# Kernel optimization log

Measured on AMD Instinct MI355X. Metric: run time of the kernel, lower is better.

The kernel has to match this reference:

```python
import jax, jax.numpy as jnp
import numpy as np

B, T, D, H, HD, FF = 1024, 128, 128, 4, 32, 512
SCALE = D ** -0.5  # NOTE: original scales by full EMBED_DIM**-0.5, not head_dim
EPS = 1e-5


def setup_inputs() -> dict:
    key = jax.random.key(0)
    ks = jax.random.split(key, 14)
    s = 0.02
    return {
        "x": jax.random.normal(ks[0], (B, T, D), dtype=jnp.float32),
        "ln1_g": jnp.ones((D,), jnp.float32),
        "ln1_b": jnp.zeros((D,), jnp.float32),
        "Wq": jax.random.normal(ks[1], (H, HD, D), jnp.float32) * s,
        "Wk": jax.random.normal(ks[2], (H, HD, D), jnp.float32) * s,
        "Wv": jax.random.normal(ks[3], (H, HD, D), jnp.float32) * s,
        "Wo": jax.random.normal(ks[4], (D, D), jnp.float32) * s,
        "bo": jnp.zeros((D,), jnp.float32),
        "ln2_g": jnp.ones((D,), jnp.float32),
        "ln2_b": jnp.zeros((D,), jnp.float32),
        "W1": jax.random.normal(ks[5], (FF, D), jnp.float32) * s,
        "b1": jnp.zeros((FF,), jnp.float32),
        "W2": jax.random.normal(ks[6], (D, FF), jnp.float32) * s,
        "b2": jnp.zeros((D,), jnp.float32),
    }


def _layer_norm(x, g, b):
    mu = jnp.mean(x, axis=-1, keepdims=True)
    var = jnp.mean(jnp.square(x - mu), axis=-1, keepdims=True)
    return (x - mu) * jax.lax.rsqrt(var + EPS) * g + b


def reference(x, ln1_g, ln1_b, Wq, Wk, Wv, Wo, bo, ln2_g, ln2_b, W1, b1, W2, b2):
    # --- attention sub-block ---
    h = _layer_norm(x, ln1_g, ln1_b)                       # [B,T,D]
    q = jnp.einsum('btd,nhd->bnth', h, Wq)                 # [B,H,T,HD]
    k = jnp.einsum('btd,nhd->bnth', h, Wk)
    v = jnp.einsum('btd,nhd->bnth', h, Wv)
    scores = jnp.einsum('bnth,bnsh->bnts', q, k) * SCALE   # [B,H,T,T]
    causal = jnp.tril(jnp.ones((T, T), dtype=bool))
    scores = jnp.where(causal, scores, -jnp.inf)
    w = jax.nn.softmax(scores, axis=-1)                    # dropout = eval identity
    attn = jnp.einsum('bnts,bnsh->bnth', w, v)             # [B,H,T,HD]
    attn = attn.transpose(0, 2, 1, 3).reshape(B, T, D)     # concat heads
    x = x + attn @ Wo.T + bo
    # --- feed-forward sub-block ---
    h2 = _layer_norm(x, ln2_g, ln2_b)
    ff = jax.nn.relu(h2 @ W1.T + b1) @ W2.T + b2
    return x + ff
```

## Files before the change

### kernel.cpp

```cpp
#include <hip/hip_runtime.h>
#include <hip/hip_bf16.h>


typedef short bf16x8 __attribute__((ext_vector_type(8)));
typedef float f32x4  __attribute__((ext_vector_type(4)));
typedef unsigned short u16;
typedef unsigned int   u32;

#define TT   128
#define DDIM 128
#define FFD  512
#define PIT  136

__device__ __forceinline__ u16 f2b(float f) {
    __hip_bfloat16 h = __float2bfloat16(f);
    return __builtin_bit_cast(u16, h);
}
__device__ __forceinline__ bf16x8 ldfrag(const u16* p) {
    return __builtin_bit_cast(bf16x8, *reinterpret_cast<const uint4*>(p));
}
__device__ __forceinline__ bf16x8 ldfrag_f32(const float* p) {
    float4 a = *reinterpret_cast<const float4*>(p);
    float4 b = *reinterpret_cast<const float4*>(p + 4);
    bf16x8 r;
    r[0] = (short)f2b(a.x); r[1] = (short)f2b(a.y);
    r[2] = (short)f2b(a.z); r[3] = (short)f2b(a.w);
    r[4] = (short)f2b(b.x); r[5] = (short)f2b(b.y);
    r[6] = (short)f2b(b.z); r[7] = (short)f2b(b.w);
    return r;
}
__device__ __forceinline__ f32x4 mfma16(bf16x8 a, bf16x8 b, f32x4 c) {
    return __builtin_amdgcn_mfma_f32_16x16x32_bf16(a, b, c, 0, 0, 0);
}

__global__ __launch_bounds__(512, 2) void tblock_kernel(
    const float* __restrict__ x,
    const float* __restrict__ ln1g, const float* __restrict__ ln1b,
    const float* __restrict__ Wq,   const float* __restrict__ Wk, const float* __restrict__ Wv,
    const float* __restrict__ Wo,   const float* __restrict__ bo,
    const float* __restrict__ ln2g, const float* __restrict__ ln2b,
    const float* __restrict__ W1,   const float* __restrict__ b1,
    const float* __restrict__ W2,   const float* __restrict__ b2,
    float* __restrict__ out)
{
    __shared__ __align__(16) u16 sm[4 * TT * PIT];
    u16* bufA = sm;
    u16* bufB = sm + 1 * TT * PIT;
    u16* bufC = sm + 2 * TT * PIT;
    u16* bufD = sm + 3 * TT * PIT;

    const int b    = blockIdx.x;
    const int tid  = threadIdx.x;
    const int w    = tid >> 6;
    const int l    = tid & 63;
    const int lq   = l & 15;
    const int quad = l >> 4;
    const float* xb = x + (size_t)b * (TT * DDIM);

    {
        const int row = tid >> 2, part = tid & 3;
        const float* src = xb + row * DDIM + part * 32;
        float v[32];
        float s = 0.f, s2 = 0.f;
        #pragma unroll
        for (int i = 0; i < 8; i++) {
            float4 u = *reinterpret_cast<const float4*>(src + i * 4);
            v[i * 4 + 0] = u.x; v[i * 4 + 1] = u.y;
            v[i * 4 + 2] = u.z; v[i * 4 + 3] = u.w;
            s  += u.x + u.y + u.z + u.w;
            s2 += u.x * u.x + u.y * u.y + u.z * u.z + u.w * u.w;
        }
        s  += __shfl_xor(s, 1);  s2 += __shfl_xor(s2, 1);
        s  += __shfl_xor(s, 2);  s2 += __shfl_xor(s2, 2);
        float mean = s * (1.f / 128.f);
        float var  = fmaxf(s2 * (1.f / 128.f) - mean * mean, 0.f);
        float rstd = rsqrtf(var + 1e-5f);
        u16* dst = bufA + row * PIT + part * 32;
        #pragma unroll
        for (int i = 0; i < 4; i++) {
            u32 o4[4];
            #pragma unroll
            for (int j = 0; j < 4; j++) {
                int c = part * 32 + i * 8 + 2 * j;
                float r0 = (v[i * 8 + 2 * j]     - mean) * rstd * ln1g[c]     + ln1b[c];
                float r1 = (v[i * 8 + 2 * j + 1] - mean) * rstd * ln1g[c + 1] + ln1b[c + 1];
                o4[j] = (u32)f2b(r0) | ((u32)f2b(r1) << 16);
            }
            uint4 pk; pk.x = o4[0]; pk.y = o4[1]; pk.z = o4[2]; pk.w = o4[3];
            *reinterpret_cast<uint4*>(dst + i * 8) = pk;
        }
    }
    __syncthreads();

    {
        bf16x8 bq[4], bk[4];
        #pragma unroll
        for (int ks = 0; ks < 4; ks++) {
            bq[ks] = ldfrag_f32(Wq + (w * 16 + lq) * DDIM + ks * 32 + quad * 8);
            bk[ks] = ldfrag_f32(Wk + (w * 16 + lq) * DDIM + ks * 32 + quad * 8);
        }
        #pragma unroll
        for (int m = 0; m < 8; m++) {
            f32x4 accq = {0, 0, 0, 0}, acck = {0, 0, 0, 0};
            #pragma unroll
            for (int ks = 0; ks < 4; ks++) {
                bf16x8 a = ldfrag(bufA + (m * 16 + lq) * PIT + ks * 32 + quad * 8);
                accq = mfma16(a, bq[ks], accq);
                acck = mfma16(a, bk[ks], acck);
            }
            #pragma unroll
            for (int r = 0; r < 4; r++) {
                int t = m * 16 + quad * 4 + r;
                bufB[t * PIT + w * 16 + lq] = f2b(accq[r]);
                bufC[t * PIT + w * 16 + lq] = f2b(acck[r]);
            }
        }
        bf16x8 av[4];
        #pragma unroll
        for (int ks = 0; ks < 4; ks++)
            av[ks] = ldfrag_f32(Wv + (w * 16 + lq) * DDIM + ks * 32 + quad * 8);
        #pragma unroll
        for (int n = 0; n < 8; n++) {
            f32x4 acc = {0, 0, 0, 0};
            #pragma unroll
            for (int ks = 0; ks < 4; ks++) {
                bf16x8 bh = ldfrag(bufA + (n * 16 + lq) * PIT + ks * 32 + quad * 8);
                acc = mfma16(av[ks], bh, acc);
            }
            #pragma unroll
            for (int r = 0; r < 4; r++) {
                int o = w * 16 + quad * 4 + r;
                bufD[o * PIT + n * 16 + lq] = f2b(acc[r]);
            }
        }
    }
    __syncthreads();

    const float SCALE = 0.08838834764831845f;
    #pragma unroll 1
    for (int h = 0; h < 4; h++) {
        bf16x8 aq = ldfrag(bufB + (w * 16 + lq) * PIT + h * 32 + quad * 8);
        float p[8][4];
        #pragma unroll
        for (int n = 0; n < 8; n++) {
            bf16x8 bk = ldfrag(bufC + (n * 16 + lq) * PIT + h * 32 + quad * 8);
            f32x4 s4 = {0, 0, 0, 0};
            s4 = mfma16(aq, bk, s4);
            #pragma unroll
            for (int r = 0; r < 4; r++) p[n][r] = s4[r];
        }
        #pragma unroll
        for (int r = 0; r < 4; r++) {
            int t = w * 16 + quad * 4 + r;
            float mx = -3.0e38f;
            #pragma unroll
            for (int n = 0; n < 8; n++) {
                int sc = n * 16 + lq;
                float val = p[n][r] * SCALE;
                p[n][r] = val;
                mx = (sc <= t) ? fmaxf(mx, val) : mx;
            }
            mx = fmaxf(mx, __shfl_xor(mx, 1));
            mx = fmaxf(mx, __shfl_xor(mx, 2));
            mx = fmaxf(mx, __shfl_xor(mx, 4));
            mx = fmaxf(mx, __shfl_xor(mx, 8));
            float sum = 0.f;
            #pragma unroll
            for (int n = 0; n < 8; n++) {
                int sc = n * 16 + lq;
                float e = (sc <= t) ? __expf(p[n][r] - mx) : 0.f;
                p[n][r] = e; sum += e;
            }
            sum += __shfl_xor(sum, 1);
            sum += __shfl_xor(sum, 2);
            sum += __shfl_xor(sum, 4);
            sum += __shfl_xor(sum, 8);
            float inv = 1.f / sum;
            #pragma unroll
            for (int n = 0; n < 8; n++)
                bufA[t * PIT + n * 16 + lq] = f2b(p[n][r] * inv);
        }
        __syncthreads();
        f32x4 o0 = {0, 0, 0, 0}, o1 = {0, 0, 0, 0};
        #pragma unroll
        for (int ks = 0; ks < 4; ks++) {
            bf16x8 ap  = ldfrag(bufA + (w * 16 + lq) * PIT + ks * 32 + quad * 8);
            bf16x8 bv0 = ldfrag(bufD + (h * 32 + lq) * PIT + ks * 32 + quad * 8);
            bf16x8 bv1 = ldfrag(bufD + (h * 32 + 16 + lq) * PIT + ks * 32 + quad * 8);
            o0 = mfma16(ap, bv0, o0);
            o1 = mfma16(ap, bv1, o1);
        }
        __syncthreads();
        #pragma unroll
        for (int r = 0; r < 4; r++) {
            int t = w * 16 + quad * 4 + r;
            bufB[t * PIT + h * 32 + lq]      = f2b(o0[r]);
            bufB[t * PIT + h * 32 + 16 + lq] = f2b(o1[r]);
        }
    }
    __syncthreads();

    float x1res[8][4];
    const int dcol = w * 16 + lq;
    {
        bf16x8 bw[4];
        #pragma unroll
        for (int ks = 0; ks < 4; ks++)
            bw[ks] = ldfrag_f32(Wo + (w * 16 + lq) * DDIM + ks * 32 + quad * 8);
        const float bov = bo[dcol];
        #pragma unroll
        for (int m = 0; m < 8; m++) {
            f32x4 acc = {0, 0, 0, 0};
            #pragma unroll
            for (int ks = 0; ks < 4; ks++) {
                bf16x8 a = ldfrag(bufB + (m * 16 + lq) * PIT + ks * 32 + quad * 8);
                acc = mfma16(a, bw[ks], acc);
            }
            #pragma unroll
            for (int r = 0; r < 4; r++) {
                int t = m * 16 + quad * 4 + r;
                float xv = xb[t * DDIM + dcol];
                float x1 = acc[r] + xv + bov;
                x1res[m][r] = x1;
                bufC[t * PIT + dcol] = f2b(x1);
            }
        }
    }
    __syncthreads();

    {
        const int row = tid >> 2, part = tid & 3;
        const u16* src = bufC + row * PIT + part * 32;
        float v[32];
        float s = 0.f, s2 = 0.f;
        #pragma unroll
        for (int i = 0; i < 4; i++) {
            uint4 u = *reinterpret_cast<const uint4*>(src + i * 8);
            u32 arr[4] = {u.x, u.y, u.z, u.w};
            #pragma unroll
            for (int j = 0; j < 4; j++) {
                float f0 = __uint_as_float((arr[j] & 0xffffu) << 16);
                float f1 = __uint_as_float(arr[j] & 0xffff0000u);
                v[i * 8 + 2 * j] = f0; v[i * 8 + 2 * j + 1] = f1;
                s += f0 + f1; s2 += f0 * f0 + f1 * f1;
            }
        }
        s  += __shfl_xor(s, 1);  s2 += __shfl_xor(s2, 1);
        s  += __shfl_xor(s, 2);  s2 += __shfl_xor(s2, 2);
        float mean = s * (1.f / 128.f);
        float var  = fmaxf(s2 * (1.f / 128.f) - mean * mean, 0.f);
        float rstd = rsqrtf(var + 1e-5f);
        u16* dst = bufD + row * PIT + part * 32;
        #pragma unroll
        for (int i = 0; i < 4; i++) {
            u32 o4[4];
            #pragma unroll
            for (int j = 0; j < 4; j++) {
                int c = part * 32 + i * 8 + 2 * j;
                float r0 = (v[i * 8 + 2 * j]     - mean) * rstd * ln2g[c]     + ln2b[c];
                float r1 = (v[i * 8 + 2 * j + 1] - mean) * rstd * ln2g[c + 1] + ln2b[c + 1];
                o4[j] = (u32)f2b(r0) | ((u32)f2b(r1) << 16);
            }
            uint4 pk; pk.x = o4[0]; pk.y = o4[1]; pk.z = o4[2]; pk.w = o4[3];
            *reinterpret_cast<uint4*>(dst + i * 8) = pk;
        }
    }
    __syncthreads();

    f32x4 oacc[8];
    #pragma unroll
    for (int m = 0; m < 8; m++) oacc[m] = f32x4{0, 0, 0, 0};

    #pragma unroll 1
    for (int fc = 0; fc < 4; fc++) {
        const int fbase = fc * 128;
        bf16x8 wf1[4];
        #pragma unroll
        for (int ks = 0; ks < 4; ks++)
            wf1[ks] = ldfrag_f32(W1 + (fbase + w * 16 + lq) * DDIM + ks * 32 + quad * 8);
        const float b1v = b1[fbase + w * 16 + lq];
        #pragma unroll
        for (int m = 0; m < 8; m++) {
            f32x4 acc = {0, 0, 0, 0};
            #pragma unroll
            for (int ks = 0; ks < 4; ks++) {
                bf16x8 a = ldfrag(bufD + (m * 16 + lq) * PIT + ks * 32 + quad * 8);
                acc = mfma16(a, wf1[ks], acc);
            }
            #pragma unroll
            for (int r = 0; r < 4; r++) {
                int t = m * 16 + quad * 4 + r;
                float g = acc[r] + b1v;
                g = g > 0.f ? g : 0.f;
                bufA[t * PIT + w * 16 + lq] = f2b(g);
            }
        }
        __syncthreads();
        bf16x8 wf2[4];
        #pragma unroll
        for (int ks = 0; ks < 4; ks++)
            wf2[ks] = ldfrag_f32(W2 + (w * 16 + lq) * FFD + fbase + ks * 32 + quad * 8);
        #pragma unroll
        for (int m = 0; m < 8; m++) {
            #pragma unroll
            for (int ks = 0; ks < 4; ks++) {
                bf16x8 a = ldfrag(bufA + (m * 16 + lq) * PIT + ks * 32 + quad * 8);
                oacc[m] = mfma16(a, wf2[ks], oacc[m]);
            }
        }
        __syncthreads();
    }

    {
        const float b2v = b2[dcol];
        float* ob = out + (size_t)b * (TT * DDIM);
        #pragma unroll
        for (int m = 0; m < 8; m++) {
            #pragma unroll
            for (int r = 0; r < 4; r++) {
                int t = m * 16 + quad * 4 + r;
                ob[t * DDIM + dcol] = oacc[m][r] + x1res[m][r] + b2v;
            }
        }
    }
}

extern "C" void kernel_launch(void* const* d_in, const int* in_sizes, int n_in,
                              void* d_out, int out_size, void* d_ws, size_t ws_size,
                              hipStream_t stream) {
    const float* x    = (const float*)d_in[0];
    const float* ln1g = (const float*)d_in[1];
    const float* ln1b = (const float*)d_in[2];
    const float* Wq   = (const float*)d_in[3];
    const float* Wk   = (const float*)d_in[4];
    const float* Wv   = (const float*)d_in[5];
    const float* Wo   = (const float*)d_in[6];
    const float* bo   = (const float*)d_in[7];
    const float* ln2g = (const float*)d_in[8];
    const float* ln2b = (const float*)d_in[9];
    const float* W1   = (const float*)d_in[10];
    const float* b1   = (const float*)d_in[11];
    const float* W2   = (const float*)d_in[12];
    const float* b2   = (const float*)d_in[13];
    float* out = (float*)d_out;

    const int nblocks = in_sizes[0] / (TT * DDIM);
    tblock_kernel<<<dim3(nblocks), dim3(512), 0, stream>>>(
        x, ln1g, ln1b, Wq, Wk, Wv, Wo, bo, ln2g, ln2b, W1, b1, W2, b2, out);
}
```

Measured before the change: 325.6 us.

## Restructure attention per-head with register-resident Q, swizzled LDS, and fused Wo

Shrinks shared memory from four padded 128x136 buffers to 64KB, using XOR-swizzled layouts instead of padding, and raises launch bounds to target more blocks per CU. Q is computed once and held in registers through a shuffle-based fragment transpose. K and V are computed per head into small LDS tiles, and the Wo projection is fused into the head loop so the concatenated attention output never goes to LDS. Softmax now uses exp2 with a prescaled Q and a hardware reciprocal, and LN2 runs directly from accumulator registers. The cost is recomputing the h fragment loads and reloading weights from global each head, plus extra shuffles and more register pressure.

```diff
diff --git a/kernel.cpp b/kernel.cpp
--- a/kernel.cpp
+++ b/kernel.cpp
@@ -10,11 +10,32 @@
 #define TT   128
 #define DDIM 128
 #define FFD  512
-#define PIT  136
+#define KPIT 40
+
+#define QSCALE 0.12751743f
+
+#if defined(__has_builtin)
+#if __has_builtin(__builtin_amdgcn_exp2f)
+#define EXP2F(x) __builtin_amdgcn_exp2f(x)
+#else
+#define EXP2F(x) exp2f(x)
+#endif
+#if __has_builtin(__builtin_amdgcn_rcpf)
+#define RCPF(x) __builtin_amdgcn_rcpf(x)
+#else
+#define RCPF(x) (1.0f / (x))
+#endif
+#else
+#define EXP2F(x) exp2f(x)
+#define RCPF(x) (1.0f / (x))
+#endif
 
 __device__ __forceinline__ u16 f2b(float f) {
     __hip_bfloat16 h = __float2bfloat16(f);
     return __builtin_bit_cast(u16, h);
+}
+__device__ __forceinline__ u32 pk2(float x, float y) {
+    return (u32)f2b(x) | ((u32)f2b(y) << 16);
 }
 __device__ __forceinline__ bf16x8 ldfrag(const u16* p) {
     return __builtin_bit_cast(bf16x8, *reinterpret_cast<const uint4*>(p));
@@ -32,8 +53,42 @@
 __device__ __forceinline__ f32x4 mfma16(bf16x8 a, bf16x8 b, f32x4 c) {
     return __builtin_amdgcn_mfma_f32_16x16x32_bf16(a, b, c, 0, 0, 0);
 }
-
-__global__ __launch_bounds__(512, 2) void tblock_kernel(
+__device__ __forceinline__ bf16x8 ld_sw(const u16* base, int row, int cg) {
+    return ldfrag(base + row * 128 + ((cg ^ (row & 7)) * 8));
+}
+__device__ __forceinline__ void st_sw(u16* base, int row, int col, u16 v) {
+    base[row * 128 + (((col >> 3) ^ (row & 7)) * 8) + (col & 7)] = v;
+}
+
+__device__ __forceinline__ void quad_collect(const float (&vals)[8][4],
+                                             bf16x8 (&fr)[4], int lane) {
+    const int srcA = (lane & 15) + ((lane & 16) << 1);
+    const int srcB = srcA + 16;
+    const bool hi = (lane & 32) != 0;
+    #pragma unroll
+    for (int g = 0; g < 4; g++) {
+        u32 D00 = pk2(vals[2*g][0],     vals[2*g][1]);
+        u32 D01 = pk2(vals[2*g][2],     vals[2*g][3]);
+        u32 D10 = pk2(vals[2*g + 1][0], vals[2*g + 1][1]);
+        u32 D11 = pk2(vals[2*g + 1][2], vals[2*g + 1][3]);
+        u32 a00 = (u32)__shfl((int)D00, srcA);
+        u32 a10 = (u32)__shfl((int)D10, srcA);
+        u32 a01 = (u32)__shfl((int)D01, srcA);
+        u32 a11 = (u32)__shfl((int)D11, srcA);
+        u32 b00 = (u32)__shfl((int)D00, srcB);
+        u32 b10 = (u32)__shfl((int)D10, srcB);
+        u32 b01 = (u32)__shfl((int)D01, srcB);
+        u32 b11 = (u32)__shfl((int)D11, srcB);
+        uint4 q;
+        q.x = hi ? a10 : a00;
+        q.y = hi ? a11 : a01;
+        q.z = hi ? b10 : b00;
+        q.w = hi ? b11 : b01;
+        fr[g] = __builtin_bit_cast(bf16x8, q);
+    }
+}
+
+__global__ __launch_bounds__(512, 4) void tblock_kernel(
     const float* __restrict__ x,
     const float* __restrict__ ln1g, const float* __restrict__ ln1b,
     const float* __restrict__ Wq,   const float* __restrict__ Wk, const float* __restrict__ Wv,
@@ -43,11 +98,12 @@
     const float* __restrict__ W2,   const float* __restrict__ b2,
     float* __restrict__ out)
 {
-    __shared__ __align__(16) u16 sm[4 * TT * PIT];
-    u16* bufA = sm;
-    u16* bufB = sm + 1 * TT * PIT;
-    u16* bufC = sm + 2 * TT * PIT;
-    u16* bufD = sm + 3 * TT * PIT;
+    __shared__ __align__(16) u16 sm[32768];
+    u16* bufH = sm;
+    u16* r2   = sm + 16384;
+    u16* Kh   = r2;
+    u16* Vth  = r2 + 5120;
+    u16* bnc  = r2 + 5120 + 4096;
 
     const int b    = blockIdx.x;
     const int tid  = threadIdx.x;
@@ -75,7 +131,6 @@
         float mean = s * (1.f / 128.f);
         float var  = fmaxf(s2 * (1.f / 128.f) - mean * mean, 0.f);
         float rstd = rsqrtf(var + 1e-5f);
-        u16* dst = bufA + row * PIT + part * 32;
         #pragma unroll
         for (int i = 0; i < 4; i++) {
             u32 o4[4];
@@ -86,190 +141,190 @@
                 float r1 = (v[i * 8 + 2 * j + 1] - mean) * rstd * ln1g[c + 1] + ln1b[c + 1];
                 o4[j] = (u32)f2b(r0) | ((u32)f2b(r1) << 16);
             }
-            uint4 pk; pk.x = o4[0]; pk.y = o4[1]; pk.z = o4[2]; pk.w = o4[3];
-            *reinterpret_cast<uint4*>(dst + i * 8) = pk;
+            uint4 pkv; pkv.x = o4[0]; pkv.y = o4[1]; pkv.z = o4[2]; pkv.w = o4[3];
+            int g = (part * 4 + i) ^ (row & 7);
+            *reinterpret_cast<uint4*>(bufH + row * 128 + g * 8) = pkv;
         }
     }
     __syncthreads();
 
+    bf16x8 qf0, qf1, qf2, qf3;
     {
-        bf16x8 bq[4], bk[4];
-        #pragma unroll
-        for (int ks = 0; ks < 4; ks++) {
-            bq[ks] = ldfrag_f32(Wq + (w * 16 + lq) * DDIM + ks * 32 + quad * 8);
-            bk[ks] = ldfrag_f32(Wk + (w * 16 + lq) * DDIM + ks * 32 + quad * 8);
-        }
-        #pragma unroll
-        for (int m = 0; m < 8; m++) {
-            f32x4 accq = {0, 0, 0, 0}, acck = {0, 0, 0, 0};
+        bf16x8 hf[4];
+        #pragma unroll
+        for (int ks = 0; ks < 4; ks++) hf[ks] = ld_sw(bufH, w * 16 + lq, ks * 4 + quad);
+        float qt[8][4];
+        #pragma unroll
+        for (int mt = 0; mt < 8; mt++) {
+            f32x4 acc = {0, 0, 0, 0};
             #pragma unroll
             for (int ks = 0; ks < 4; ks++) {
-                bf16x8 a = ldfrag(bufA + (m * 16 + lq) * PIT + ks * 32 + quad * 8);
-                accq = mfma16(a, bq[ks], accq);
-                acck = mfma16(a, bk[ks], acck);
-            }
-            #pragma unroll
-            for (int r = 0; r < 4; r++) {
-                int t = m * 16 + quad * 4 + r;
-                bufB[t * PIT + w * 16 + lq] = f2b(accq[r]);
-                bufC[t * PIT + w * 16 + lq] = f2b(acck[r]);
-            }
-        }
-        bf16x8 av[4];
-        #pragma unroll
-        for (int ks = 0; ks < 4; ks++)
-            av[ks] = ldfrag_f32(Wv + (w * 16 + lq) * DDIM + ks * 32 + quad * 8);
-        #pragma unroll
-        for (int n = 0; n < 8; n++) {
-            f32x4 acc = {0, 0, 0, 0};
-            #pragma unroll
-            for (int ks = 0; ks < 4; ks++) {
-                bf16x8 bh = ldfrag(bufA + (n * 16 + lq) * PIT + ks * 32 + quad * 8);
-                acc = mfma16(av[ks], bh, acc);
-            }
-            #pragma unroll
-            for (int r = 0; r < 4; r++) {
-                int o = w * 16 + quad * 4 + r;
-                bufD[o * PIT + n * 16 + lq] = f2b(acc[r]);
-            }
-        }
-    }
-    __syncthreads();
-
-    const float SCALE = 0.08838834764831845f;
+                bf16x8 a = ldfrag_f32(Wq + (mt * 16 + lq) * DDIM + ks * 32 + quad * 8);
+                acc = mfma16(a, hf[ks], acc);
+            }
+            #pragma unroll
+            for (int r = 0; r < 4; r++) qt[mt][r] = acc[r] * QSCALE;
+        }
+        bf16x8 qfr[4];
+        quad_collect(qt, qfr, l);
+        qf0 = qfr[0]; qf1 = qfr[1]; qf2 = qfr[2]; qf3 = qfr[3];
+    }
+
+    f32x4 x1acc[8];
+    #pragma unroll
+    for (int i = 0; i < 8; i++) x1acc[i] = f32x4{0, 0, 0, 0};
+
     #pragma unroll 1
     for (int h = 0; h < 4; h++) {
-        bf16x8 aq = ldfrag(bufB + (w * 16 + lq) * PIT + h * 32 + quad * 8);
+        {
+            bf16x8 hf[4];
+            #pragma unroll
+            for (int ks = 0; ks < 4; ks++) hf[ks] = ld_sw(bufH, w * 16 + lq, ks * 4 + quad);
+            #pragma unroll
+            for (int nt2 = 0; nt2 < 2; nt2++) {
+                f32x4 acc = {0, 0, 0, 0};
+                #pragma unroll
+                for (int ks = 0; ks < 4; ks++) {
+                    bf16x8 bwk = ldfrag_f32(Wk + (h * 32 + nt2 * 16 + lq) * DDIM + ks * 32 + quad * 8);
+                    acc = mfma16(hf[ks], bwk, acc);
+                }
+                #pragma unroll
+                for (int r = 0; r < 4; r++)
+                    Kh[(w * 16 + quad * 4 + r) * KPIT + nt2 * 16 + lq] = f2b(acc[r]);
+            }
+        }
+        {
+            bf16x8 af[4];
+            #pragma unroll
+            for (int ks = 0; ks < 4; ks++)
+                af[ks] = ldfrag_f32(Wv + (h * 32 + (w >> 2) * 16 + lq) * DDIM + ks * 32 + quad * 8);
+            #pragma unroll
+            for (int j2 = 0; j2 < 2; j2++) {
+                int nt = 2 * (w & 3) + j2;
+                f32x4 acc = {0, 0, 0, 0};
+                #pragma unroll
+                for (int ks = 0; ks < 4; ks++) {
+                    bf16x8 bh = ld_sw(bufH, nt * 16 + lq, ks * 4 + quad);
+                    acc = mfma16(af[ks], bh, acc);
+                }
+                #pragma unroll
+                for (int r = 0; r < 4; r++)
+                    st_sw(Vth, (w >> 2) * 16 + quad * 4 + r, nt * 16 + lq, f2b(acc[r]));
+            }
+        }
+        __syncthreads();
+
+        bf16x8 qh = (h == 0) ? qf0 : (h == 1) ? qf1 : (h == 2) ? qf2 : qf3;
         float p[8][4];
         #pragma unroll
-        for (int n = 0; n < 8; n++) {
-            bf16x8 bk = ldfrag(bufC + (n * 16 + lq) * PIT + h * 32 + quad * 8);
-            f32x4 s4 = {0, 0, 0, 0};
-            s4 = mfma16(aq, bk, s4);
-            #pragma unroll
-            for (int r = 0; r < 4; r++) p[n][r] = s4[r];
-        }
+        for (int ns = 0; ns < 8; ns++) {
+            bf16x8 a = ldfrag(Kh + (ns * 16 + lq) * KPIT + quad * 8);
+            f32x4 s4 = mfma16(a, qh, f32x4{0, 0, 0, 0});
+            #pragma unroll
+            for (int r = 0; r < 4; r++) p[ns][r] = s4[r];
+        }
+        const int trow = w * 16 + lq;
+        float mx = -3.0e38f;
+        #pragma unroll
+        for (int ns = 0; ns < 8; ns++) {
+            #pragma unroll
+            for (int r = 0; r < 4; r++) {
+                int sidx = ns * 16 + quad * 4 + r;
+                mx = (sidx <= trow) ? fmaxf(mx, p[ns][r]) : mx;
+            }
+        }
+        mx = fmaxf(mx, __shfl_xor(mx, 16));
+        mx = fmaxf(mx, __shfl_xor(mx, 32));
+        float sum = 0.f;
+        #pragma unroll
+        for (int ns = 0; ns < 8; ns++) {
+            #pragma unroll
+            for (int r = 0; r < 4; r++) {
+                int sidx = ns * 16 + quad * 4 + r;
+                float e = (sidx <= trow) ? EXP2F(p[ns][r] - mx) : 0.f;
+                p[ns][r] = e; sum += e;
+            }
+        }
+        sum += __shfl_xor(sum, 16);
+        sum += __shfl_xor(sum, 32);
+        float inv = RCPF(sum);
+        #pragma unroll
+        for (int ns = 0; ns < 8; ns++)
+            #pragma unroll
+            for (int r = 0; r < 4; r++) p[ns][r] *= inv;
+
+        bf16x8 pfr[4];
+        quad_collect(p, pfr, l);
+        f32x4 av0 = {0, 0, 0, 0}, av1 = {0, 0, 0, 0};
+        #pragma unroll
+        for (int ks = 0; ks < 4; ks++) {
+            int g8 = ((ks * 4 + quad) ^ (lq & 7)) * 8;
+            av0 = mfma16(pfr[ks], ldfrag(Vth + lq * 128 + g8), av0);
+            av1 = mfma16(pfr[ks], ldfrag(Vth + (16 + lq) * 128 + g8), av1);
+        }
+        u16* bw_ = bnc + w * (16 * KPIT);
         #pragma unroll
         for (int r = 0; r < 4; r++) {
-            int t = w * 16 + quad * 4 + r;
-            float mx = -3.0e38f;
-            #pragma unroll
-            for (int n = 0; n < 8; n++) {
-                int sc = n * 16 + lq;
-                float val = p[n][r] * SCALE;
-                p[n][r] = val;
-                mx = (sc <= t) ? fmaxf(mx, val) : mx;
-            }
-            mx = fmaxf(mx, __shfl_xor(mx, 1));
-            mx = fmaxf(mx, __shfl_xor(mx, 2));
-            mx = fmaxf(mx, __shfl_xor(mx, 4));
-            mx = fmaxf(mx, __shfl_xor(mx, 8));
-            float sum = 0.f;
-            #pragma unroll
-            for (int n = 0; n < 8; n++) {
-                int sc = n * 16 + lq;
-                float e = (sc <= t) ? __expf(p[n][r] - mx) : 0.f;
-                p[n][r] = e; sum += e;
-            }
-            sum += __shfl_xor(sum, 1);
-            sum += __shfl_xor(sum, 2);
-            sum += __shfl_xor(sum, 4);
-            sum += __shfl_xor(sum, 8);
-            float inv = 1.f / sum;
-            #pragma unroll
-            for (int n = 0; n < 8; n++)
-                bufA[t * PIT + n * 16 + lq] = f2b(p[n][r] * inv);
+            bw_[(quad * 4 + r) * KPIT + lq]      = f2b(av0[r]);
+            bw_[(quad * 4 + r) * KPIT + 16 + lq] = f2b(av1[r]);
+        }
+        asm volatile("s_waitcnt lgkmcnt(0)" ::: "memory");
+        __builtin_amdgcn_sched_barrier(0);
+        bf16x8 pa = ldfrag(bw_ + lq * KPIT + quad * 8);
+        #pragma unroll
+        for (int nt = 0; nt < 8; nt++) {
+            bf16x8 wo = ldfrag_f32(Wo + (nt * 16 + lq) * DDIM + h * 32 + quad * 8);
+            x1acc[nt] = mfma16(pa, wo, x1acc[nt]);
         }
         __syncthreads();
-        f32x4 o0 = {0, 0, 0, 0}, o1 = {0, 0, 0, 0};
-        #pragma unroll
-        for (int ks = 0; ks < 4; ks++) {
-            bf16x8 ap  = ldfrag(bufA + (w * 16 + lq) * PIT + ks * 32 + quad * 8);
-            bf16x8 bv0 = ldfrag(bufD + (h * 32 + lq) * PIT + ks * 32 + quad * 8);
-            bf16x8 bv1 = ldfrag(bufD + (h * 32 + 16 + lq) * PIT + ks * 32 + quad * 8);
-            o0 = mfma16(ap, bv0, o0);
-            o1 = mfma16(ap, bv1, o1);
-        }
-        __syncthreads();
+    }
+
+    #pragma unroll
+    for (int nt = 0; nt < 8; nt++) {
+        float bov = bo[nt * 16 + lq];
+        #pragma unroll
+        for (int r = 0; r < 4; r++)
+            x1acc[nt][r] += xb[(w * 16 + quad * 4 + r) * DDIM + nt * 16 + lq] + bov;
+    }
+
+    {
+        float s[4] = {0, 0, 0, 0}, s2[4] = {0, 0, 0, 0};
+        #pragma unroll
+        for (int nt = 0; nt < 8; nt++) {
+            #pragma unroll
+            for (int r = 0; r < 4; r++) {
+                float v = x1acc[nt][r];
+                s[r] += v; s2[r] += v * v;
+            }
+        }
+        float mean_[4], rstd_[4];
         #pragma unroll
         for (int r = 0; r < 4; r++) {
-            int t = w * 16 + quad * 4 + r;
-            bufB[t * PIT + h * 32 + lq]      = f2b(o0[r]);
-            bufB[t * PIT + h * 32 + 16 + lq] = f2b(o1[r]);
-        }
-    }
-    __syncthreads();
-
-    float x1res[8][4];
-    const int dcol = w * 16 + lq;
-    {
-        bf16x8 bw[4];
-        #pragma unroll
-        for (int ks = 0; ks < 4; ks++)
-            bw[ks] = ldfrag_f32(Wo + (w * 16 + lq) * DDIM + ks * 32 + quad * 8);
-        const float bov = bo[dcol];
-        #pragma unroll
-        for (int m = 0; m < 8; m++) {
-            f32x4 acc = {0, 0, 0, 0};
-            #pragma unroll
-            for (int ks = 0; ks < 4; ks++) {
-                bf16x8 a = ldfrag(bufB + (m * 16 + lq) * PIT + ks * 32 + quad * 8);
-                acc = mfma16(a, bw[ks], acc);
-            }
-            #pragma unroll
-            for (int r = 0; r < 4; r++) {
-                int t = m * 16 + quad * 4 + r;
-                float xv = xb[t * DDIM + dcol];
-                float x1 = acc[r] + xv + bov;
-                x1res[m][r] = x1;
-                bufC[t * PIT + dcol] = f2b(x1);
-            }
-        }
-    }
-    __syncthreads();
-
-    {
-        const int row = tid >> 2, part = tid & 3;
-        const u16* src = bufC + row * PIT + part * 32;
-        float v[32];
-        float s = 0.f, s2 = 0.f;
-        #pragma unroll
-        for (int i = 0; i < 4; i++) {
-            uint4 u = *reinterpret_cast<const uint4*>(src + i * 8);
-            u32 arr[4] = {u.x, u.y, u.z, u.w};
-            #pragma unroll
-            for (int j = 0; j < 4; j++) {
-                float f0 = __uint_as_float((arr[j] & 0xffffu) << 16);
-                float f1 = __uint_as_float(arr[j] & 0xffff0000u);
-                v[i * 8 + 2 * j] = f0; v[i * 8 + 2 * j + 1] = f1;
-                s += f0 + f1; s2 += f0 * f0 + f1 * f1;
-            }
-        }
-        s  += __shfl_xor(s, 1);  s2 += __shfl_xor(s2, 1);
-        s  += __shfl_xor(s, 2);  s2 += __shfl_xor(s2, 2);
-        float mean = s * (1.f / 128.f);
-        float var  = fmaxf(s2 * (1.f / 128.f) - mean * mean, 0.f);
-        float rstd = rsqrtf(var + 1e-5f);
-        u16* dst = bufD + row * PIT + part * 32;
-        #pragma unroll
-        for (int i = 0; i < 4; i++) {
-            u32 o4[4];
-            #pragma unroll
-            for (int j = 0; j < 4; j++) {
-                int c = part * 32 + i * 8 + 2 * j;
-                float r0 = (v[i * 8 + 2 * j]     - mean) * rstd * ln2g[c]     + ln2b[c];
-                float r1 = (v[i * 8 + 2 * j + 1] - mean) * rstd * ln2g[c + 1] + ln2b[c + 1];
-                o4[j] = (u32)f2b(r0) | ((u32)f2b(r1) << 16);
-            }
-            uint4 pk; pk.x = o4[0]; pk.y = o4[1]; pk.z = o4[2]; pk.w = o4[3];
-            *reinterpret_cast<uint4*>(dst + i * 8) = pk;
+            #pragma unroll
+            for (int m_ = 1; m_ <= 8; m_ <<= 1) {
+                s[r]  += __shfl_xor(s[r],  m_);
+                s2[r] += __shfl_xor(s2[r], m_);
+            }
+            mean_[r] = s[r] * (1.f / 128.f);
+            float var = fmaxf(s2[r] * (1.f / 128.f) - mean_[r] * mean_[r], 0.f);
+            rstd_[r] = rsqrtf(var + 1e-5f);
+        }
+        #pragma unroll
+        for (int nt = 0; nt < 8; nt++) {
+            int d = nt * 16 + lq;
+            float gg = ln2g[d], bb = ln2b[d];
+            #pragma unroll
+            for (int r = 0; r < 4; r++) {
+                int t2 = w * 16 + quad * 4 + r;
+                st_sw(bufH, t2, d, f2b((x1acc[nt][r] - mean_[r]) * rstd_[r] * gg + bb));
+            }
         }
     }
     __syncthreads();
 
     f32x4 oacc[8];
     #pragma unroll
-    for (int m = 0; m < 8; m++) oacc[m] = f32x4{0, 0, 0, 0};
+    for (int i = 0; i < 8; i++) oacc[i] = f32x4{0, 0, 0, 0};
 
     #pragma unroll 1
     for (int fc = 0; fc < 4; fc++) {
@@ -283,16 +338,14 @@
         for (int m = 0; m < 8; m++) {
             f32x4 acc = {0, 0, 0, 0};
             #pragma unroll
-            for (int ks = 0; ks < 4; ks++) {
-                bf16x8 a = ldfrag(bufD + (m * 16 + lq) * PIT + ks * 32 + quad * 8);
-                acc = mfma16(a, wf1[ks], acc);
-            }
-            #pragma unroll
-            for (int r = 0; r < 4; r++) {
-                int t = m * 16 + quad * 4 + r;
-                float g = acc[r] + b1v;
-                g = g > 0.f ? g : 0.f;
-                bufA[t * PIT + w * 16 + lq] = f2b(g);
+            for (int ks = 0; ks < 4; ks++)
+                acc = mfma16(ld_sw(bufH, m * 16 + lq, ks * 4 + quad), wf1[ks], acc);
+            #pragma unroll
+            for (int r = 0; r < 4; r++) {
+                int t2 = m * 16 + quad * 4 + r;
+                float gv = acc[r] + b1v;
+                gv = gv > 0.f ? gv : 0.f;
+                st_sw(r2, t2, w * 16 + lq, f2b(gv));
             }
         }
         __syncthreads();
@@ -303,23 +356,28 @@
         #pragma unroll
         for (int m = 0; m < 8; m++) {
             #pragma unroll
-            for (int ks = 0; ks < 4; ks++) {
-                bf16x8 a = ldfrag(bufA + (m * 16 + lq) * PIT + ks * 32 + quad * 8);
-                oacc[m] = mfma16(a, wf2[ks], oacc[m]);
-            }
+            for (int ks = 0; ks < 4; ks++)
+                oacc[m] = mfma16(ld_sw(r2, m * 16 + lq, ks * 4 + quad), wf2[ks], oacc[m]);
         }
         __syncthreads();
     }
 
+    float* x1f = reinterpret_cast<float*>(sm);
+    #pragma unroll
+    for (int nt = 0; nt < 8; nt++)
+        #pragma unroll
+        for (int r = 0; r < 4; r++)
+            x1f[(w * 16 + quad * 4 + r) * 128 + nt * 16 + lq] = x1acc[nt][r];
+    __syncthreads();
     {
-        const float b2v = b2[dcol];
+        const float b2v = b2[w * 16 + lq];
         float* ob = out + (size_t)b * (TT * DDIM);
         #pragma unroll
         for (int m = 0; m < 8; m++) {
             #pragma unroll
             for (int r = 0; r < 4; r++) {
-                int t = m * 16 + quad * 4 + r;
-                ob[t * DDIM + dcol] = oacc[m][r] + x1res[m][r] + b2v;
+                int t2 = m * 16 + quad * 4 + r;
+                ob[t2 * DDIM + w * 16 + lq] = oacc[m][r] + x1f[t2 * 128 + w * 16 + lq] + b2v;
             }
         }
     }
```

Result: slower. 486.8 us (+49.5%).
